# Performance work log

Measured on AMD Instinct MI355X. Metric: run time of the kernel, lower is better.

Reference implementation:

```python
import jax, jax.numpy as jnp
import numpy as np


def _samx_row(qqq, kkk, vvv):
    """Suffix-automaton qkv retrieval over binary alphabet {0,1}.
    Faithful port of samx_qkv_slow, with dict transitions replaced by two
    flat transition arrays (alphabet size is 2 after the >0 binarization).
    """
    n = len(qqq)
    y = [0] * n
    s = 2 * n + 1
    tr = [[-1] * s, [-1] * s]   # tr[sym][state] = next state, -1 = absent
    f = [-1] * s                # suffix links
    m = [0] * s                 # max length of state
    r = [-1] * s                # last end position seen
    g = 0                       # last state
    u = 1                       # next free state id
    w = 0                       # current match state (query side)
    h = 0                       # current match length
    for i in range(n):
        q = qqq[i]
        k = kkk[i]
        tq = tr[q]
        tk = tr[k]
        # --- query: extend match with symbol q, following suffix links ---
        p, x = w, h
        while p != -1 and tq[p] == -1:
            if x > m[p]:
                x = m[p]
            p = f[p]
        if p != -1:
            p, x = tq[p], x + 1
        else:
            p, x = 0, 0
        # find tightest state for match length x
        vst = p
        while f[vst] != -1 and m[f[vst]] >= x:
            vst = f[vst]
        # back off to a state with positive length and a recorded endpos
        while vst != -1 and (m[vst] <= 0 or r[vst] < 0):
            vst = f[vst]
        yi = vvv[r[vst] + 1] if vst != -1 else -1
        y[i] = yi if yi > 0 else 0
        w, h = p, x
        # --- key: standard suffix-automaton extension with symbol k ---
        j = u
        u += 1
        m[j] = m[g] + 1
        p = g
        while p != -1 and tk[p] == -1:
            tk[p] = j
            p = f[p]
        if p == -1:
            f[j] = 0
        else:
            d = tk[p]
            if m[p] + 1 == m[d]:
                f[j] = d
            else:
                b = u
                u += 1
                tr[0][b] = tr[0][d]
                tr[1][b] = tr[1][d]
                m[b] = m[p] + 1
                f[b] = f[d]
                r[b] = r[d]
                f[d] = b
                f[j] = b
                while p != -1 and tk[p] == d:
                    tk[p] = b
                    p = f[p]
        # propagate latest end position up the suffix-link chain
        vst = g = j
        while vst != -1 and r[vst] < i:
            r[vst] = i
            vst = f[vst]
    return y


def _samx_idx(q, k, v):
    """q,k,v: float arrays [b,t,c] -> int idx [b,t,c] in {0,1}."""
    b, t, c = q.shape
    qb = (np.asarray(q) > 0).astype(np.uint8).transpose(0, 2, 1).reshape(-1, t)
    kb = (np.asarray(k) > 0).astype(np.uint8).transpose(0, 2, 1).reshape(-1, t)
    vb = (np.asarray(v) > 0).astype(np.uint8).transpose(0, 2, 1).reshape(-1, t)
    rows = [_samx_row(qq.tolist(), kk.tolist(), vv.tolist())
            for qq, kk, vv in zip(qb, kb, vb)]
    idx = np.asarray(rows, dtype=np.uint8).reshape(b, c, t).transpose(0, 2, 1)
    return idx


def setup_inputs() -> dict:
    key = jax.random.key(0)
    kq, kk, kv = jax.random.split(key, 3)
    B, T, C = 4, 2048, 256
    q = jax.random.normal(kq, (B, T, C), dtype=jnp.float32)
    k = jax.random.normal(kk, (B, T, C), dtype=jnp.float32)
    v = jax.random.normal(kv, (B, T, C), dtype=jnp.float32)
    e = jnp.ones((1, 1, C), dtype=jnp.float32)
    return {"q": q, "k": k, "v": v, "e": e}


def reference(q, k, v, e):
    # Irregular pointer-chasing part runs on host (numpy); output scaling in jnp.
    idx = _samx_idx(q, k, v)                      # [b,t,c] in {0,1}
    sign = 2.0 * jnp.asarray(idx, dtype=q.dtype) - 1.0
    return sign * e
```

## Files before the change

kernel.cpp:

```cpp
#include <hip/hip_runtime.h>


#define NSTATES 4096
#define TLEN 2048

typedef unsigned long long u64m;

__global__ __launch_bounds__(64)
void samx_main(const float* __restrict__ q,
               const float* __restrict__ k,
               unsigned* __restrict__ outpos,
               int T, int C) {
  __shared__ unsigned short tr0a[NSTATES];
  __shared__ unsigned short tr1a[NSTATES];
  __shared__ unsigned       flml[NSTATES];
  __shared__ unsigned short rla[NSTATES];

  const int row = blockIdx.x;
  const int b = row / C;
  const int c = row - b * C;
  const int lane = threadIdx.x;

  for (int s = lane; s < NSTATES; s += 64) {
    tr0a[s] = 0xFFFFu; tr1a[s] = 0xFFFFu;
    flml[s] = 0x0000FFFFu; rla[s] = 0xFFFFu;
  }

  const size_t rowbase = (size_t)b * (size_t)T * (size_t)C + (size_t)c;
  const float* qr = q + rowbase;
  const float* kr = k + rowbase;
  unsigned* outr = outpos + rowbase;

  unsigned qw = 0u, kw = 0u;
  {
    const int t0 = lane * 32;
#pragma unroll 8
    for (int jj = 0; jj < 32; ++jj) {
      const int t = t0 + jj;
      if (qr[(size_t)t * C] > 0.0f) qw |= (1u << jj);
      if (kr[(size_t)t * C] > 0.0f) kw |= (1u << jj);
    }
  }
  __syncthreads();

  int cid = 0;
  bool cval = (lane == 0);
  bool trunc = false;

  int g = 0;
  int mlg = 0;
  int u = 1;
  int w = 0;
  int h = 0;

  int qs = (int)(__builtin_amdgcn_readlane((int)qw, 0) & 1);
  int ks = (int)(__builtin_amdgcn_readlane((int)kw, 0) & 1);
  unsigned short* tq = qs ? tr1a : tr0a;
  unsigned short* tk = ks ? tr1a : tr0a;
  int      pf_img = (int)(short)tk[cid];
  unsigned pf_fm  = flml[cid];
  int      pf_t1  = (int)(short)tq[w];
  unsigned pf_fm1 = flml[w];

  for (int i = 0; i < T; ++i) {
    const bool hot = !trunc;
    const int img  = pf_img;
    const int myml = (int)(pf_fm >> 16);

    const int j = u++;
    const int mlj = mlg + 1;

    int d = -1, bb = -1, flj = 0, ndd = 0, newlen = 2, pushed = 0;
    unsigned fmd = 0;
    bool prefl = false, inrun = false;

    if (hot) {
      const u64m brkmask = __ballot(cval && img != -1);
      const bool nobrk = (brkmask == 0);
      const int t2 = nobrk ? 64 : (int)__builtin_ctzll(brkmask);
      const int t2c = (t2 > 63) ? 63 : t2;
      d = __builtin_amdgcn_readlane(img, t2c);
      const int mlp = __builtin_amdgcn_readlane(myml, t2c);
      const int dld = (d < 0) ? 0 : d;
      prefl = cval && (lane < t2);

      fmd = flml[dld];
      int dtr0 = (int)(short)tr0a[dld];
      int dtr1 = (int)(short)tr1a[dld];
      int lm1 = lane - 1; if (lm1 < 0) lm1 = 0;
      const int previmg = __builtin_amdgcn_ds_bpermute(lm1 << 2, img);

      if (!nobrk) {
        const int mld = (int)(fmd >> 16);
        if (mlp + 1 == mld) {
          flj = d;
        } else {
          bb = u++;
          const u64m pb = __ballot(prefl && cid == d);
          if (pb != 0ull) { if (ks) dtr1 = j; else dtr0 = j; }
          if (lane == 0) {
            tr0a[bb] = (unsigned short)dtr0;
            tr1a[bb] = (unsigned short)dtr1;
            flml[bb] = (fmd & 0xFFFFu) | ((unsigned)(mlp + 1) << 16);
          }
          flj = bb;
        }
      }
      if (lane == 0)
        flml[j] = (unsigned)(flj & 0xFFFF) | ((unsigned)mlj << 16);

      if (bb >= 0) {
        const u64m eq = __ballot(cval && img == d) >> t2;
        const int runlen = (eq == ~0ull) ? 64 : (int)__builtin_ctzll(~eq);
        inrun = cval && lane >= t2 && lane < t2 + runlen;
      }
      const bool rs = cval && lane >= t2 && (lane == t2 || img != previmg);
      const u64m rsmask = __ballot(rs);
      ndd = (int)__builtin_popcountll(rsmask);
      newlen = ndd + 2;
      const unsigned below =
          __builtin_amdgcn_mbcnt_hi((unsigned)(rsmask >> 32),
              __builtin_amdgcn_mbcnt_lo((unsigned)rsmask, 0u));
      const int dst = rs ? ((int)below + 1) : 0;
      pushed = __builtin_amdgcn_ds_permute(dst << 2, img);
    }

    int p = w, x = h;
    {
      int tv = pf_t1; unsigned fm = pf_fm1;
      for (;;) {
        if (p == -1) { p = 0; x = 0; break; }
        if (tv != -1) { p = tv; x = x + 1; break; }
        const int mp = (int)(fm >> 16);
        if (x > mp) x = mp;
        p = (int)(short)(fm & 0xFFFFu);
        if (p == -1) { p = 0; x = 0; break; }
        tv = (int)(short)tq[p]; fm = flml[p];
      }
    }

    int vst = p;
    unsigned fmv = flml[vst];
    for (;;) {
      const int fv = (int)(short)(fmv & 0xFFFFu);
      if (fv == -1) break;
      const unsigned fmf = flml[fv];
      if ((int)(fmf >> 16) < x) break;
      vst = fv; fmv = fmf;
    }
    int rv = -1;
    for (;;) {
      if (vst == -1) { rv = -1; break; }
      const unsigned fm2 = flml[vst];
      const int r2 = (int)(short)rla[vst];
      if ((int)(fm2 >> 16) > 0 && r2 >= 0) { rv = r2; break; }
      vst = (int)(short)(fm2 & 0xFFFFu);
    }
    w = p; h = x;

    if (hot) {
      if (prefl) tk[cid] = (unsigned short)j;
      if (inrun) tk[cid] = (unsigned short)bb;
      if (bb >= 0 && lane == 0)
        flml[d] = (fmd & 0xFFFF0000u) | (unsigned)bb;
      if (lane == 0) outr[(size_t)i * C] = (unsigned)(rv + 1);

      int nv = 0;
      if (lane == 0) nv = j;
      else if (lane == 1) nv = flj;
      else if (lane - 1 < ndd) nv = pushed;
      const bool nval = (lane < newlen);
      if (nval) rla[nv] = (unsigned short)i;

      const bool overflow = (newlen > 64);
      if (overflow) {
        const int nv63 = __builtin_amdgcn_readlane(nv, 63);
        if (lane == 0) {
          int vp = (int)(short)(flml[nv63] & 0xFFFFu);
          while (vp != -1) {
            rla[vp] = (unsigned short)i;
            vp = (int)(short)(flml[vp] & 0xFFFFu);
          }
        }
      }
      cid = nv; cval = nval; trunc = overflow;
    } else {
      int pcur = g, d2 = -1, idbrk = -1;
      for (;;) {
        if (pcur == -1) break;
        const int tv = (int)(short)tk[pcur];
        const unsigned fm = flml[pcur];
        if (tv != -1) { d2 = tv; idbrk = pcur; break; }
        if (lane == 0) tk[pcur] = (unsigned short)j;
        pcur = (int)(short)(fm & 0xFFFFu);
      }
      int fl2 = 0;
      if (d2 != -1) {
        const int mlp = (int)(flml[idbrk] >> 16);
        const unsigned fmd2 = flml[d2];
        const int mld = (int)(fmd2 >> 16);
        if (mlp + 1 == mld) {
          fl2 = d2;
        } else {
          const int bbc = u++;
          const int dtr0 = (int)(short)tr0a[d2];
          const int dtr1 = (int)(short)tr1a[d2];
          const int drl  = (int)(short)rla[d2];
          if (lane == 0) {
            tr0a[bbc] = (unsigned short)dtr0;
            tr1a[bbc] = (unsigned short)dtr1;
            rla[bbc]  = (unsigned short)drl;
            flml[bbc] = (fmd2 & 0xFFFFu) | ((unsigned)(mlp + 1) << 16);
            flml[d2]  = (fmd2 & 0xFFFF0000u) | (unsigned)bbc;
          }
          fl2 = bbc;
          int p3 = idbrk;
          for (;;) {
            if (p3 == -1) break;
            const int tv3 = (int)(short)tk[p3];
            const unsigned fm3 = flml[p3];
            if (tv3 != d2) break;
            if (lane == 0) tk[p3] = (unsigned short)bbc;
            p3 = (int)(short)(fm3 & 0xFFFFu);
          }
        }
      }
      if (lane == 0) {
        flml[j] = (unsigned)(fl2 & 0xFFFF) | ((unsigned)mlj << 16);
        outr[(size_t)i * C] = (unsigned)(rv + 1);
      }
      int vp = j, ncs = 0;
      bool tr2 = false;
      for (;;) {
        if (vp == -1) break;
        if (ncs < 64) { if (lane == ncs) cid = vp; ++ncs; }
        else tr2 = true;
        if (lane == 0) rla[vp] = (unsigned short)i;
        vp = (int)(short)(flml[vp] & 0xFFFFu);
      }
      cval = (lane < ncs);
      trunc = tr2;
    }
    g = j; mlg = mlj;

    if (i + 1 < T) {
      const int in = i + 1;
      const unsigned qwn = (unsigned)__builtin_amdgcn_readlane((int)qw, in >> 5);
      const unsigned kwn = (unsigned)__builtin_amdgcn_readlane((int)kw, in >> 5);
      qs = (int)((qwn >> (in & 31)) & 1u);
      ks = (int)((kwn >> (in & 31)) & 1u);
      tq = qs ? tr1a : tr0a;
      tk = ks ? tr1a : tr0a;
      pf_img = (int)(short)tk[cid];
      pf_fm  = flml[cid];
      pf_t1  = (int)(short)tq[w];
      pf_fm1 = flml[w];
    }
  }
}

__global__ __launch_bounds__(256)
void samx_epilogue(const float* __restrict__ v,
                   const float* __restrict__ e,
                   unsigned* __restrict__ out,
                   int T, int C, int total) {
  const int idx = blockIdx.x * 256 + threadIdx.x;
  if (idx >= total) return;
  const unsigned vidx = out[idx];
  const int c = idx % C;
  const int bi = idx / C;
  const int b = bi / T;
  const float ev = e[c];
  float val = -ev;
  if (vidx != 0u) {
    if (v[((size_t)b * (size_t)T + (size_t)vidx) * (size_t)C + (size_t)c] > 0.0f)
      val = ev;
  }
  out[idx] = __float_as_uint(val);
}

extern "C" void kernel_launch(void* const* d_in, const int* in_sizes, int n_in,
                              void* d_out, int out_size, void* d_ws, size_t ws_size,
                              hipStream_t stream) {
  const float* q = (const float*)d_in[0];
  const float* k = (const float*)d_in[1];
  const float* v = (const float*)d_in[2];
  const float* e = (const float*)d_in[3];

  const int C = in_sizes[3];
  const int T = TLEN;
  const int B = in_sizes[0] / (T * C);
  const int total = out_size;

  samx_main<<<dim3(B * C), dim3(64), 0, stream>>>(q, k, (unsigned*)d_out, T, C);
  samx_epilogue<<<dim3((total + 255) / 256), dim3(256), 0, stream>>>(
      v, e, (unsigned*)d_out, T, C, total);
}
```

Measured before the change: 1.960 ms.

## Pack SAM state fields into one 64-bit LDS record per state

Merges the two transition arrays and the packed link/length array into a single 64-bit record per state, so one LDS load fetches both transitions, the suffix link and the max length. The query-side record for the current match state is now carried in a register and patched with the wave's own updates, instead of being reloaded each step. The serial pointer-chasing loops are meant to issue fewer dependent LDS loads per step. In exchange the code carries more bit-extraction arithmetic and extra ballots to keep the cached record consistent, which is a correctness risk if any update path is missed.

```diff
diff --git a/kernel.cpp b/kernel.cpp
--- a/kernel.cpp
+++ b/kernel.cpp
@@ -5,16 +5,27 @@
 #define TLEN 2048
 
 typedef unsigned long long u64m;
+
+__device__ __forceinline__ int f_tr(u64m r, int s) {
+  return (int)(short)(unsigned short)(r >> (s << 4));
+}
+__device__ __forceinline__ int f_fl(u64m r) {
+  return (int)(short)(unsigned short)(r >> 32);
+}
+__device__ __forceinline__ int f_ml(u64m r) {
+  return (int)(r >> 48);
+}
 
 __global__ __launch_bounds__(64)
 void samx_main(const float* __restrict__ q,
                const float* __restrict__ k,
                unsigned* __restrict__ outpos,
                int T, int C) {
-  __shared__ unsigned short tr0a[NSTATES];
-  __shared__ unsigned short tr1a[NSTATES];
-  __shared__ unsigned       flml[NSTATES];
+  __shared__ u64m           reca[NSTATES];
   __shared__ unsigned short rla[NSTATES];
+
+  unsigned short* recw = (unsigned short*)reca;
+  unsigned*       rech = (unsigned*)reca;
 
   const int row = blockIdx.x;
   const int b = row / C;
@@ -22,8 +33,8 @@
   const int lane = threadIdx.x;
 
   for (int s = lane; s < NSTATES; s += 64) {
-    tr0a[s] = 0xFFFFu; tr1a[s] = 0xFFFFu;
-    flml[s] = 0x0000FFFFu; rla[s] = 0xFFFFu;
+    reca[s] = 0x0000FFFFFFFFFFFFull;
+    rla[s] = 0xFFFFu;
   }
 
   const size_t rowbase = (size_t)b * (size_t)T * (size_t)C + (size_t)c;
@@ -55,23 +66,19 @@
 
   int qs = (int)(__builtin_amdgcn_readlane((int)qw, 0) & 1);
   int ks = (int)(__builtin_amdgcn_readlane((int)kw, 0) & 1);
-  unsigned short* tq = qs ? tr1a : tr0a;
-  unsigned short* tk = ks ? tr1a : tr0a;
-  int      pf_img = (int)(short)tk[cid];
-  unsigned pf_fm  = flml[cid];
-  int      pf_t1  = (int)(short)tq[w];
-  unsigned pf_fm1 = flml[w];
+  u64m pf_rec = reca[0];
+  u64m recp   = pf_rec;
 
   for (int i = 0; i < T; ++i) {
     const bool hot = !trunc;
-    const int img  = pf_img;
-    const int myml = (int)(pf_fm >> 16);
+    const u64m rk  = pf_rec;
+    const int img  = f_tr(rk, ks);
+    const int myml = f_ml(rk);
 
     const int j = u++;
     const int mlj = mlg + 1;
 
     int d = -1, bb = -1, flj = 0, ndd = 0, newlen = 2, pushed = 0;
-    unsigned fmd = 0;
     bool prefl = false, inrun = false;
 
     if (hot) {
@@ -84,30 +91,32 @@
       const int dld = (d < 0) ? 0 : d;
       prefl = cval && (lane < t2);
 
-      fmd = flml[dld];
-      int dtr0 = (int)(short)tr0a[dld];
-      int dtr1 = (int)(short)tr1a[dld];
+      const u64m recd = reca[dld];
       int lm1 = lane - 1; if (lm1 < 0) lm1 = 0;
       const int previmg = __builtin_amdgcn_ds_bpermute(lm1 << 2, img);
 
+      const unsigned fmdhi = (unsigned)(recd >> 32);
       if (!nobrk) {
-        const int mld = (int)(fmd >> 16);
+        const int mld = (int)(fmdhi >> 16);
         if (mlp + 1 == mld) {
           flj = d;
         } else {
           bb = u++;
+          int dtr0 = f_tr(recd, 0);
+          int dtr1 = f_tr(recd, 1);
           const u64m pb = __ballot(prefl && cid == d);
           if (pb != 0ull) { if (ks) dtr1 = j; else dtr0 = j; }
           if (lane == 0) {
-            tr0a[bb] = (unsigned short)dtr0;
-            tr1a[bb] = (unsigned short)dtr1;
-            flml[bb] = (fmd & 0xFFFFu) | ((unsigned)(mlp + 1) << 16);
+            reca[bb] = (u64m)(unsigned short)dtr0
+                     | ((u64m)(unsigned short)dtr1 << 16)
+                     | ((u64m)(fmdhi & 0xFFFFu) << 32)
+                     | ((u64m)(unsigned)(mlp + 1) << 48);
           }
           flj = bb;
         }
       }
       if (lane == 0)
-        flml[j] = (unsigned)(flj & 0xFFFF) | ((unsigned)mlj << 16);
+        rech[2 * j + 1] = (unsigned)(flj & 0xFFFF) | ((unsigned)mlj << 16);
 
       if (bb >= 0) {
         const u64m eq = __ballot(cval && img == d) >> t2;
@@ -127,43 +136,57 @@
 
     int p = w, x = h;
     {
-      int tv = pf_t1; unsigned fm = pf_fm1;
+      u64m rr = recp;
       for (;;) {
         if (p == -1) { p = 0; x = 0; break; }
+        const int tv = f_tr(rr, qs);
         if (tv != -1) { p = tv; x = x + 1; break; }
-        const int mp = (int)(fm >> 16);
+        const int mp = f_ml(rr);
         if (x > mp) x = mp;
-        p = (int)(short)(fm & 0xFFFFu);
+        p = f_fl(rr);
         if (p == -1) { p = 0; x = 0; break; }
-        tv = (int)(short)tq[p]; fm = flml[p];
-      }
-    }
-
+        rr = reca[p];
+      }
+    }
+
+    const u64m recP = reca[p];
+    int rlv = (int)(short)rla[p];
+    unsigned fmv = (unsigned)(recP >> 32);
     int vst = p;
-    unsigned fmv = flml[vst];
     for (;;) {
       const int fv = (int)(short)(fmv & 0xFFFFu);
       if (fv == -1) break;
-      const unsigned fmf = flml[fv];
+      const unsigned fmf = rech[2 * fv + 1];
+      const int rlf = (int)(short)rla[fv];
       if ((int)(fmf >> 16) < x) break;
-      vst = fv; fmv = fmf;
+      vst = fv; fmv = fmf; rlv = rlf;
     }
     int rv = -1;
     for (;;) {
       if (vst == -1) { rv = -1; break; }
-      const unsigned fm2 = flml[vst];
-      const int r2 = (int)(short)rla[vst];
-      if ((int)(fm2 >> 16) > 0 && r2 >= 0) { rv = r2; break; }
-      vst = (int)(short)(fm2 & 0xFFFFu);
+      if ((int)(fmv >> 16) > 0 && rlv >= 0) { rv = rlv; break; }
+      vst = (int)(short)(fmv & 0xFFFFu);
+      if (vst == -1) { rv = -1; break; }
+      fmv = rech[2 * vst + 1];
+      rlv = (int)(short)rla[vst];
     }
     w = p; h = x;
 
     if (hot) {
-      if (prefl) tk[cid] = (unsigned short)j;
-      if (inrun) tk[cid] = (unsigned short)bb;
-      if (bb >= 0 && lane == 0)
-        flml[d] = (fmd & 0xFFFF0000u) | (unsigned)bb;
+      if (prefl) recw[4 * cid + ks] = (unsigned short)j;
+      if (inrun) recw[4 * cid + ks] = (unsigned short)bb;
+      if (bb >= 0 && lane == 0) recw[4 * d + 2] = (unsigned short)bb;
       if (lane == 0) outr[(size_t)i * C] = (unsigned)(rv + 1);
+
+      u64m rp = recP;
+      if (bb >= 0 && p == d)
+        rp = (rp & ~(0xFFFFull << 32)) | ((u64m)(unsigned short)bb << 32);
+      const int sh = ks << 4;
+      if (__ballot(prefl && cid == p) != 0ull)
+        rp = (rp & ~(0xFFFFull << sh)) | ((u64m)(unsigned short)j << sh);
+      if (__ballot(inrun && cid == p) != 0ull)
+        rp = (rp & ~(0xFFFFull << sh)) | ((u64m)(unsigned short)bb << sh);
+      recp = rp;
 
       int nv = 0;
       if (lane == 0) nv = j;
@@ -176,10 +199,10 @@
       if (overflow) {
         const int nv63 = __builtin_amdgcn_readlane(nv, 63);
         if (lane == 0) {
-          int vp = (int)(short)(flml[nv63] & 0xFFFFu);
+          int vp = (int)(short)(rech[2 * nv63 + 1] & 0xFFFFu);
           while (vp != -1) {
             rla[vp] = (unsigned short)i;
-            vp = (int)(short)(flml[vp] & 0xFFFFu);
+            vp = (int)(short)(rech[2 * vp + 1] & 0xFFFFu);
           }
         }
       }
@@ -188,45 +211,44 @@
       int pcur = g, d2 = -1, idbrk = -1;
       for (;;) {
         if (pcur == -1) break;
-        const int tv = (int)(short)tk[pcur];
-        const unsigned fm = flml[pcur];
+        const u64m rr = reca[pcur];
+        const int tv = f_tr(rr, ks);
         if (tv != -1) { d2 = tv; idbrk = pcur; break; }
-        if (lane == 0) tk[pcur] = (unsigned short)j;
-        pcur = (int)(short)(fm & 0xFFFFu);
+        if (lane == 0) recw[4 * pcur + ks] = (unsigned short)j;
+        pcur = f_fl(rr);
       }
       int fl2 = 0;
       if (d2 != -1) {
-        const int mlp = (int)(flml[idbrk] >> 16);
-        const unsigned fmd2 = flml[d2];
-        const int mld = (int)(fmd2 >> 16);
-        if (mlp + 1 == mld) {
+        const int mlp2 = f_ml(reca[idbrk]);
+        const u64m rd2 = reca[d2];
+        const int mld = f_ml(rd2);
+        if (mlp2 + 1 == mld) {
           fl2 = d2;
         } else {
           const int bbc = u++;
-          const int dtr0 = (int)(short)tr0a[d2];
-          const int dtr1 = (int)(short)tr1a[d2];
-          const int drl  = (int)(short)rla[d2];
+          const int drl = (int)(short)rla[d2];
           if (lane == 0) {
-            tr0a[bbc] = (unsigned short)dtr0;
-            tr1a[bbc] = (unsigned short)dtr1;
-            rla[bbc]  = (unsigned short)drl;
-            flml[bbc] = (fmd2 & 0xFFFFu) | ((unsigned)(mlp + 1) << 16);
-            flml[d2]  = (fmd2 & 0xFFFF0000u) | (unsigned)bbc;
+            reca[bbc] = (u64m)(unsigned short)f_tr(rd2, 0)
+                      | ((u64m)(unsigned short)f_tr(rd2, 1) << 16)
+                      | ((u64m)((unsigned)(rd2 >> 32) & 0xFFFFu) << 32)
+                      | ((u64m)(unsigned)(mlp2 + 1) << 48);
+            rla[bbc] = (unsigned short)drl;
+            recw[4 * d2 + 2] = (unsigned short)bbc;
           }
           fl2 = bbc;
           int p3 = idbrk;
           for (;;) {
             if (p3 == -1) break;
-            const int tv3 = (int)(short)tk[p3];
-            const unsigned fm3 = flml[p3];
+            const u64m r3 = reca[p3];
+            const int tv3 = f_tr(r3, ks);
             if (tv3 != d2) break;
-            if (lane == 0) tk[p3] = (unsigned short)bbc;
-            p3 = (int)(short)(fm3 & 0xFFFFu);
+            if (lane == 0) recw[4 * p3 + ks] = (unsigned short)bbc;
+            p3 = f_fl(r3);
           }
         }
       }
       if (lane == 0) {
-        flml[j] = (unsigned)(fl2 & 0xFFFF) | ((unsigned)mlj << 16);
+        rech[2 * j + 1] = (unsigned)(fl2 & 0xFFFF) | ((unsigned)mlj << 16);
         outr[(size_t)i * C] = (unsigned)(rv + 1);
       }
       int vp = j, ncs = 0;
@@ -236,25 +258,21 @@
         if (ncs < 64) { if (lane == ncs) cid = vp; ++ncs; }
         else tr2 = true;
         if (lane == 0) rla[vp] = (unsigned short)i;
-        vp = (int)(short)(flml[vp] & 0xFFFFu);
+        vp = (int)(short)(rech[2 * vp + 1] & 0xFFFFu);
       }
       cval = (lane < ncs);
       trunc = tr2;
+      recp = reca[w];
     }
     g = j; mlg = mlj;
 
     if (i + 1 < T) {
+      pf_rec = reca[cid];
       const int in = i + 1;
       const unsigned qwn = (unsigned)__builtin_amdgcn_readlane((int)qw, in >> 5);
       const unsigned kwn = (unsigned)__builtin_amdgcn_readlane((int)kw, in >> 5);
       qs = (int)((qwn >> (in & 31)) & 1u);
       ks = (int)((kwn >> (in & 31)) & 1u);
-      tq = qs ? tr1a : tr0a;
-      tk = ks ? tr1a : tr0a;
-      pf_img = (int)(short)tk[cid];
-      pf_fm  = flml[cid];
-      pf_t1  = (int)(short)tq[w];
-      pf_fm1 = flml[w];
     }
   }
 }
```

Measured after the change: 1.987 ms. About the same (+1.4%).
